# Performance work log

Hardware: AMD Instinct MI355X
Metric: run time of the kernel (lower is better)

## Reference

```python
import jax, jax.numpy as jnp
import numpy as np

DIM = 128
HEADS = 4
GN_GROUPS = 4
EPS = 1e-5


def setup_inputs() -> dict:
    key = jax.random.key(0)
    ks = jax.random.split(key, 6)
    B, C, H, W = 4, DIM, 64, 64
    x = jax.random.normal(ks[0], (B, C, H, W), dtype=jnp.float32)
    # 1x1 convs are channel matmuls: store as [out_ch, in_ch]
    w_qkv = jax.random.normal(ks[1], (3 * C, C), dtype=jnp.float32) * (C ** -0.5)
    w_out = jax.random.normal(ks[2], (C, C), dtype=jnp.float32) * (C ** -0.5)
    b_out = jax.random.normal(ks[3], (C,), dtype=jnp.float32) * 0.01
    gn_gamma = jnp.ones((C,), dtype=jnp.float32)
    gn_beta = jnp.zeros((C,), dtype=jnp.float32)
    return {"x": x, "w_qkv": w_qkv, "w_out": w_out, "b_out": b_out,
            "gn_gamma": gn_gamma, "gn_beta": gn_beta}


def _attention_block(x, w_qkv, w_out, b_out, gn_gamma, gn_beta):
    b, c, h, w = x.shape
    d = c // HEADS
    scale = d ** -0.5
    # 1x1 conv == per-pixel matmul over channels
    qkv = jnp.einsum('bchw,oc->bohw', x, w_qkv)  # [b, 3c, h, w]
    q, k, v = jnp.split(qkv, 3, axis=1)
    # 'b (h d) x y -> b h (x y) d'
    def to_heads(t):
        return t.reshape(b, HEADS, d, h * w).transpose(0, 1, 3, 2)  # [b, H, N, d]
    q, k, v = to_heads(q), to_heads(k), to_heads(v)
    dots = jnp.einsum('bhnd,bhmd->bhnm', q, k) * scale  # [b, H, N, N]
    attn = jax.nn.softmax(dots, axis=-1)
    out = jnp.einsum('bhnm,bhmd->bhnd', attn, v)  # [b, H, N, d]
    # 'b h (x y) d -> b (h d) x y'
    out = out.transpose(0, 1, 3, 2).reshape(b, c, h, w)
    # output 1x1 conv + bias
    out = jnp.einsum('bchw,oc->bohw', out, w_out) + b_out[None, :, None, None]
    # GroupNorm(4, c)
    g = out.reshape(b, GN_GROUPS, c // GN_GROUPS, h, w)
    mean = g.mean(axis=(2, 3, 4), keepdims=True)
    var = g.var(axis=(2, 3, 4), keepdims=True)
    g = (g - mean) * jax.lax.rsqrt(var + EPS)
    out = g.reshape(b, c, h, w) * gn_gamma[None, :, None, None] + gn_beta[None, :, None, None]
    return out + x


def reference(x, w_qkv, w_out, b_out, gn_gamma, gn_beta):
    return _attention_block(x, w_qkv, w_out, b_out, gn_gamma, gn_beta)
```

## Files before the change

### kernel.cpp

```cpp
#include <hip/hip_runtime.h>

#define DIM   128
#define NPIX  4096
#define DHEAD 32

using u16 = unsigned short;
typedef __attribute__((ext_vector_type(8))) short   short8;
typedef __attribute__((ext_vector_type(8))) u16     ushort8;
typedef __attribute__((ext_vector_type(4))) float   floatx4;
typedef __attribute__((ext_vector_type(2))) unsigned int uint2v;

#define SCL 0.25513899f

__device__ __forceinline__ float bf2f(u16 u) {
  union { unsigned int i; float f; } v; v.i = ((unsigned int)u) << 16; return v.f;
}
__device__ __forceinline__ u16 f2bf(float f) {
  union { unsigned int i; float f; } v; v.f = f;
  unsigned int i = v.i;
  return (u16)((i + 0x7FFFu + ((i >> 16) & 1u)) >> 16);
}
__device__ __forceinline__ unsigned int pk2bf(float a, float b) {
  union { float f; unsigned int u; } ua, ub; ua.f = a; ub.f = b;
  return __builtin_amdgcn_perm(ub.u, ua.u, 0x07060302u);
}

template<bool F32> __device__ __forceinline__ float ld1(const void* p, size_t i) {
  if constexpr (F32) return ((const float*)p)[i];
  else               return bf2f(((const u16*)p)[i]);
}
template<bool F32> __device__ __forceinline__ float4 ld4(const void* p, size_t i) {
  if constexpr (F32) {
    return *(const float4*)((const float*)p + i);
  } else {
    const ushort4 u = *(const ushort4*)((const u16*)p + i);
    return make_float4(bf2f(u.x), bf2f(u.y), bf2f(u.z), bf2f(u.w));
  }
}
template<bool F32> __device__ __forceinline__ void st4(void* p, size_t i, float4 v) {
  if constexpr (F32) {
    *(float4*)((float*)p + i) = v;
  } else {
    ushort4 u; u.x = f2bf(v.x); u.y = f2bf(v.y); u.z = f2bf(v.z); u.w = f2bf(v.w);
    *(ushort4*)((u16*)p + i) = u;
  }
}

__global__ void k_detect(const u16* __restrict__ x, int* __restrict__ flag,
                         float* __restrict__ S) {
  if (threadIdx.x < 40) S[threadIdx.x] = 0.f;
  if (threadIdx.x == 0 && blockIdx.x == 0) {
    int big = 0;
    for (int i = 0; i < 128; ++i) {
      const float v = bf2f(x[i]);
      if (!(fabsf(v) < 1e4f)) big = 1;
    }
    *flag = big;
  }
}

template<bool F32>
__global__ __launch_bounds__(256) void k_qkv(const void* __restrict__ x,
                                             const void* __restrict__ wqkv,
                                             u16* __restrict__ Q,
                                             u16* __restrict__ K,
                                             u16* __restrict__ V,
                                             const int* __restrict__ flag) {
  if (*flag != (F32 ? 1 : 0)) return;
  const int b = blockIdx.z, y = blockIdx.y, pt = blockIdx.x;
  const int tl = threadIdx.x;
  __shared__ float Ws[32 * 129];
  if (y < 8) {
    const int m = y >> 2, h = y & 3;
    const int ddq = tl & 3, pw = tl >> 2;
    const int rb = m * DIM + h * 32;
    for (int i = tl; i < 32 * DIM; i += 256)
      Ws[(i >> 7) * 129 + (i & 127)] =
          ld1<F32>(wqkv, (size_t)(rb + (i >> 7)) * DIM + (i & 127));
    __syncthreads();
    const int p0 = pt * 256 + pw * 4;
    float acc[8][4];
#pragma unroll
    for (int j = 0; j < 8; ++j) { acc[j][0] = acc[j][1] = acc[j][2] = acc[j][3] = 0.f; }
    const size_t xb = (size_t)b * DIM * NPIX + p0;
    for (int c = 0; c < DIM; ++c) {
      const float4 xv = ld4<F32>(x, xb + (size_t)c * NPIX);
#pragma unroll
      for (int j = 0; j < 8; ++j) {
        const float wv = Ws[(ddq * 8 + j) * 129 + c];
        acc[j][0] += wv * xv.x; acc[j][1] += wv * xv.y;
        acc[j][2] += wv * xv.z; acc[j][3] += wv * xv.w;
      }
    }
    u16* dst = (m == 0) ? Q : K;
    const float scl = (m == 0) ? 1.f : SCL;
    const int bh = b * 4 + h;
#pragma unroll
    for (int t = 0; t < 4; ++t) {
      ushort8 w8;
#pragma unroll
      for (int j = 0; j < 8; ++j) w8[j] = f2bf(acc[j][t] * scl);
      *(ushort8*)(dst + ((size_t)bh * NPIX + p0 + t) * DHEAD + ddq * 8) = w8;
    }
  } else {
    const int og = (y - 8) * 4 + (pt >> 2);
    const int ptv = pt & 3;
    for (int i = tl; i < 8 * DIM; i += 256)
      Ws[(i >> 7) * 129 + (i & 127)] =
          ld1<F32>(wqkv, (size_t)(2 * DIM + og * 8 + (i >> 7)) * DIM + (i & 127));
    __syncthreads();
    const int p0 = ptv * 1024 + tl * 4;
    float acc[8][4];
#pragma unroll
    for (int j = 0; j < 8; ++j) { acc[j][0] = acc[j][1] = acc[j][2] = acc[j][3] = 0.f; }
    const size_t xb = (size_t)b * DIM * NPIX + p0;
    for (int c = 0; c < DIM; ++c) {
      const float4 xv = ld4<F32>(x, xb + (size_t)c * NPIX);
#pragma unroll
      for (int j = 0; j < 8; ++j) {
        const float wv = Ws[j * 129 + c];
        acc[j][0] += wv * xv.x; acc[j][1] += wv * xv.y;
        acc[j][2] += wv * xv.z; acc[j][3] += wv * xv.w;
      }
    }
#pragma unroll
    for (int j = 0; j < 8; ++j) {
      const int c = og * 8 + j;
      ushort4 w4;
      w4.x = f2bf(acc[j][0]); w4.y = f2bf(acc[j][1]);
      w4.z = f2bf(acc[j][2]); w4.w = f2bf(acc[j][3]);
      *(ushort4*)(V + ((size_t)b * DIM + c) * NPIX + p0) = w4;
    }
  }
}

__device__ __forceinline__ short8 xform_p(unsigned c0, unsigned c1,
                                          unsigned c2, unsigned c3) {
  uint2v sw = __builtin_amdgcn_permlane32_swap(c0, c2, false, false);
  uint2v sx = __builtin_amdgcn_permlane16_swap(sw[0], sw[1], false, false);
  uint2v sy = __builtin_amdgcn_permlane32_swap(c1, c3, false, false);
  uint2v sz = __builtin_amdgcn_permlane16_swap(sy[0], sy[1], false, false);
  union { unsigned u[4]; short8 s; } r;
  r.u[0] = sx[0]; r.u[1] = sz[0]; r.u[2] = sx[1]; r.u[3] = sz[1];
  return r.s;
}

__global__ __launch_bounds__(512) void k_attn(const u16* __restrict__ Q,
                                              const u16* __restrict__ K,
                                              const u16* __restrict__ V,
                                              u16* __restrict__ O) {
  const int id = blockIdx.y * 32 + blockIdx.x;
  const int nid = (id & 7) * 64 + (id >> 3);
  const int bh = nid >> 5, qb = nid & 31;
  const int tid = threadIdx.x;
  const int wv = tid >> 6, lane = tid & 63;
  const int quad = lane >> 4, l15 = lane & 15;
  const int b = bh >> 2, h = bh & 3;

  __shared__ __align__(16) u16 Klds[2][128 * 40];
  __shared__ __align__(16) u16 Vlds[2][32 * 136];
  __shared__ __align__(16) u16 Olds[32 * 136];

  const int qtok0 = qb * 128 + wv * 16 + l15;
  const short8 qf = *(const short8*)(Q + ((size_t)bh * NPIX + qtok0) * DHEAD + quad * 8);

  floatx4 o00 = {0.f, 0.f, 0.f, 0.f}, o01 = {0.f, 0.f, 0.f, 0.f};
  floatx4 ol  = {0.f, 0.f, 0.f, 0.f};
  const short8 onesf = {(short)0x3F80, (short)0x3F80, (short)0x3F80, (short)0x3F80,
                        (short)0x3F80, (short)0x3F80, (short)0x3F80, (short)0x3F80};

  const int st = tid & 255;
  const bool isK = tid < 256;
  const int skey = st >> 2, sqt = st & 3;
  const int sdd = st >> 3, soc = st & 7;
  const u16* Gg = isK ? (K + ((size_t)bh * NPIX + skey) * DHEAD + sqt * 8)
                      : (V + ((size_t)(b * DIM + h * DHEAD + sdd)) * NPIX + soc * 8);
  u16* Ld0 = isK ? (Klds[0] + skey * 40 + sqt * 8) : (Vlds[0] + sdd * 136 + soc * 8);
  u16* Ld1 = isK ? (Klds[1] + skey * 40 + sqt * 8) : (Vlds[1] + sdd * 136 + soc * 8);
  const size_t gstep = isK ? (size_t)(128 * DHEAD) : (size_t)128;
  const size_t goff2 = isK ? (size_t)(64 * DHEAD)  : (size_t)64;
  const int    loff2 = isK ? (64 * 40) : 64;

  *(ushort8*)Ld0           = *(const ushort8*)Gg;
  *(ushort8*)(Ld0 + loff2) = *(const ushort8*)(Gg + goff2);

  for (int ch = 0; ch < 32; ++ch) {
    const int cur = ch & 1;
    __syncthreads();
    ushort8 pre0, pre1;
    if (ch + 1 < 32) {
      const u16* gb = Gg + (size_t)(ch + 1) * gstep;
      pre0 = *(const ushort8*)gb;
      pre1 = *(const ushort8*)(gb + goff2);
    }
#pragma unroll
    for (int kc = 0; kc < 4; ++kc) {
      unsigned ca[4];
#pragma unroll
      for (int s = 0; s < 2; ++s) {
        const int sub = kc * 2 + s;
        const short8 af = *(const short8*)(Klds[cur] + (sub * 16 + l15) * 40 + quad * 8);
        const floatx4 s0 = __builtin_amdgcn_mfma_f32_16x16x32_bf16(
            af, qf, (floatx4){0.f, 0.f, 0.f, 0.f}, 0, 0, 0);
        const float a0 = __builtin_amdgcn_exp2f(s0[0]);
        const float a1 = __builtin_amdgcn_exp2f(s0[1]);
        const float a2 = __builtin_amdgcn_exp2f(s0[2]);
        const float a3 = __builtin_amdgcn_exp2f(s0[3]);
        ca[s * 2 + 0] = pk2bf(a0, a1); ca[s * 2 + 1] = pk2bf(a2, a3);
      }
      const short8 pa = xform_p(ca[0], ca[1], ca[2], ca[3]);
      const short8 vb0 = *(const short8*)(Vlds[cur] + l15 * 136 + kc * 32 + quad * 8);
      const short8 vb1 = *(const short8*)(Vlds[cur] + (16 + l15) * 136 + kc * 32 + quad * 8);
      __builtin_amdgcn_s_setprio(1);
      o00 = __builtin_amdgcn_mfma_f32_16x16x32_bf16(pa, vb0, o00, 0, 0, 0);
      o01 = __builtin_amdgcn_mfma_f32_16x16x32_bf16(pa, vb1, o01, 0, 0, 0);
      ol  = __builtin_amdgcn_mfma_f32_16x16x32_bf16(pa, onesf, ol, 0, 0, 0);
      __builtin_amdgcn_s_setprio(0);
    }
    if (ch + 1 < 32) {
      u16* dst = cur ? Ld0 : Ld1;
      *(ushort8*)dst           = pre0;
      *(ushort8*)(dst + loff2) = pre1;
    }
  }
  float li[4];
#pragma unroll
  for (int r = 0; r < 4; ++r) li[r] = 1.f / ol[r];
  uint2v w00, w01;
  w00[0] = (unsigned)f2bf(o00[0] * li[0]) | ((unsigned)f2bf(o00[1] * li[1]) << 16);
  w00[1] = (unsigned)f2bf(o00[2] * li[2]) | ((unsigned)f2bf(o00[3] * li[3]) << 16);
  w01[0] = (unsigned)f2bf(o01[0] * li[0]) | ((unsigned)f2bf(o01[1] * li[1]) << 16);
  w01[1] = (unsigned)f2bf(o01[2] * li[2]) | ((unsigned)f2bf(o01[3] * li[3]) << 16);
  __syncthreads();
  *(uint2v*)(Olds + l15 * 136 + wv * 16 + quad * 4) = w00;
  *(uint2v*)(Olds + (16 + l15) * 136 + wv * 16 + quad * 4) = w01;
  __syncthreads();
  const int d = tid >> 4, oc = tid & 15;
  u16* og = O + ((size_t)(b * DIM + h * DHEAD + d)) * NPIX + qb * 128;
  *(ushort8*)(og + oc * 8) = *(const ushort8*)(Olds + d * 136 + oc * 8);
}

template<bool F32>
__global__ __launch_bounds__(256) void k_proj(const u16* __restrict__ O,
                                              const void* __restrict__ wout,
                                              const void* __restrict__ bout,
                                              float* __restrict__ Y,
                                              float* __restrict__ Sred,
                                              const int* __restrict__ flag) {
  if (*flag != (F32 ? 1 : 0)) return;
  const int b = blockIdx.z, og = blockIdx.y, pt = blockIdx.x;
  const int tl = threadIdx.x;
  __shared__ float Ws[8][DIM];
  __shared__ __align__(16) u16 Olds[2][16][520];
  for (int i = tl; i < 8 * DIM; i += 256)
    Ws[i >> 7][i & 127] = ld1<F32>(wout, (size_t)(og * 8 + (i >> 7)) * DIM + (i & 127));
  const u16* Ob = O + (size_t)b * DIM * NPIX + pt * 512;
  const int srow = tl >> 6;
  const int scol = (tl & 63) * 8;
#pragma unroll
  for (int s = 0; s < 4; ++s) {
    const int r = s * 4 + srow;
    *(ushort8*)(&Olds[0][r][scol]) = *(const ushort8*)(Ob + (size_t)r * NPIX + scol);
  }
  float acc[8][2];
#pragma unroll
  for (int j = 0; j < 8; ++j) { acc[j][0] = acc[j][1] = 0.f; }
  for (int chv = 0; chv < 8; ++chv) {
    const int cur = chv & 1;
    __syncthreads();
    ushort8 pre[4];
    if (chv + 1 < 8) {
      const u16* gb = Ob + (size_t)(chv + 1) * 16 * NPIX;
#pragma unroll
      for (int s = 0; s < 4; ++s)
        pre[s] = *(const ushort8*)(gb + (size_t)(s * 4 + srow) * NPIX + scol);
    }
#pragma unroll
    for (int cc = 0; cc < 16; ++cc) {
      const int c = chv * 16 + cc;
      const ushort2 xv2 = *(const ushort2*)(&Olds[cur][cc][tl * 2]);
      const float x0 = bf2f(xv2.x), x1 = bf2f(xv2.y);
#pragma unroll
      for (int j = 0; j < 8; ++j) {
        const float wv = Ws[j][c];
        acc[j][0] += wv * x0; acc[j][1] += wv * x1;
      }
    }
    if (chv + 1 < 8) {
      const int nxt = cur ^ 1;
#pragma unroll
      for (int s = 0; s < 4; ++s)
        *(ushort8*)(&Olds[nxt][s * 4 + srow][scol]) = pre[s];
    }
  }
  const int p0 = pt * 512 + tl * 2;
  float s1 = 0.f, s2 = 0.f;
#pragma unroll
  for (int j = 0; j < 8; ++j) {
    const int o = og * 8 + j;
    const float bo = ld1<F32>(bout, o);
    float2 y2;
    y2.x = acc[j][0] + bo; y2.y = acc[j][1] + bo;
    *(float2*)(Y + ((size_t)b * DIM + o) * NPIX + p0) = y2;
    s1 += y2.x + y2.y;
    s2 += y2.x * y2.x + y2.y * y2.y;
  }
  __shared__ float red[2][256];
  red[0][tl] = s1; red[1][tl] = s2;
  __syncthreads();
  for (int off = 128; off >= 1; off >>= 1) {
    if (tl < off) { red[0][tl] += red[0][tl + off]; red[1][tl] += red[1][tl + off]; }
    __syncthreads();
  }
  if (tl == 0) {
    const int g = og >> 2;
    atomicAdd(&Sred[(b * 4 + g) * 2 + 0], red[0][0]);
    atomicAdd(&Sred[(b * 4 + g) * 2 + 1], red[1][0]);
  }
}

template<bool F32>
__global__ __launch_bounds__(256) void k_gn(const float* __restrict__ Y,
                                            const float* __restrict__ Sred,
                                            const void* __restrict__ x,
                                            const void* __restrict__ gamma,
                                            const void* __restrict__ beta,
                                            void* __restrict__ out,
                                            const int* __restrict__ flag) {
  if (*flag != (F32 ? 1 : 0)) return;
  const int idx = (blockIdx.x * 256 + threadIdx.x) * 4;
  const int b = idx >> 19;
  const int c = (idx >> 12) & 127;
  const int g = c >> 5;
  const float inv_n = 1.f / (32.f * 4096.f);
  const float s1 = Sred[(b * 4 + g) * 2 + 0];
  const float s2 = Sred[(b * 4 + g) * 2 + 1];
  const float mean = s1 * inv_n;
  const float var = s2 * inv_n - mean * mean;
  const float rs = rsqrtf(var + 1e-5f);
  const float ga = ld1<F32>(gamma, c) * rs;
  const float be = ld1<F32>(beta, c) - mean * ga;
  const float4 y4 = *(const float4*)(Y + idx);
  const float4 xv = ld4<F32>(x, idx);
  float4 r;
  r.x = y4.x * ga + be + xv.x;
  r.y = y4.y * ga + be + xv.y;
  r.z = y4.z * ga + be + xv.z;
  r.w = y4.w * ga + be + xv.w;
  st4<F32>(out, idx, r);
}

extern "C" void kernel_launch(void* const* d_in, const int* in_sizes, int n_in,
                              void* d_out, int out_size, void* d_ws, size_t ws_size,
                              hipStream_t stream) {
  const void* x     = d_in[0];
  const void* wqkv  = d_in[1];
  const void* wout  = d_in[2];
  const void* bout  = d_in[3];
  const void* gamma = d_in[4];
  const void* beta  = d_in[5];
  char* ws = (char*)d_ws;
  u16*   Q = (u16*)(ws + ((size_t)0  << 20));
  u16*   K = (u16*)(ws + ((size_t)8  << 20));
  u16*   V = (u16*)(ws + ((size_t)16 << 20));
  u16*   O = (u16*)(ws + ((size_t)24 << 20));
  float* Y = (float*)(ws + ((size_t)32 << 20));
  float* S = (float*)(ws + ((size_t)40 << 20));
  int*   F = (int*)(ws + ((size_t)40 << 20) + 128);

  k_detect<<<1, 64, 0, stream>>>((const u16*)x, F, S);

  k_qkv<false><<<dim3(16, 12, 4), 256, 0, stream>>>(x, wqkv, Q, K, V, F);
  k_qkv<true> <<<dim3(16, 12, 4), 256, 0, stream>>>(x, wqkv, Q, K, V, F);
  k_attn<<<dim3(32, 16), 512, 0, stream>>>(Q, K, V, O);
  k_proj<false><<<dim3(8, 16, 4), 256, 0, stream>>>(O, wout, bout, Y, S, F);
  k_proj<true> <<<dim3(8, 16, 4), 256, 0, stream>>>(O, wout, bout, Y, S, F);
  k_gn<false><<<2048, 256, 0, stream>>>(Y, S, x, gamma, beta, d_out, F);
  k_gn<true> <<<2048, 256, 0, stream>>>(Y, S, x, gamma, beta, d_out, F);
}
```

Baseline: 178.5 us.

## Use MFMA bf16 tiles with double-buffered LDS staging for QKV projection

For the bf16 input path, the QKV 1x1-conv kernel now computes each 32-output by 256-pixel tile with 16x16x32 bf16 MFMA instructions instead of scalar FMAs. Weights and x are staged in padded LDS, and the next channel chunk is prefetched into registers while the current one is consumed, in a two-buffer scheme. The f32 path keeps the old scalar code. This targets the ALU cost of the projection, but the epilogue uses narrower scattered stores for V, and the grid mapping (blockIdx.y as output tile) must match the host launch, which is not shown.

Result: no change. 179.5 us (+0.5%).

```diff
diff --git a/kernel.cpp b/kernel.cpp
--- a/kernel.cpp
+++ b/kernel.cpp
@@ -67,69 +67,160 @@
                                              u16* __restrict__ V,
                                              const int* __restrict__ flag) {
   if (*flag != (F32 ? 1 : 0)) return;
-  const int b = blockIdx.z, y = blockIdx.y, pt = blockIdx.x;
+  __shared__ __align__(16) char smem[41728];
   const int tl = threadIdx.x;
-  __shared__ float Ws[32 * 129];
-  if (y < 8) {
-    const int m = y >> 2, h = y & 3;
-    const int ddq = tl & 3, pw = tl >> 2;
-    const int rb = m * DIM + h * 32;
-    for (int i = tl; i < 32 * DIM; i += 256)
-      Ws[(i >> 7) * 129 + (i & 127)] =
-          ld1<F32>(wqkv, (size_t)(rb + (i >> 7)) * DIM + (i & 127));
+  if constexpr (F32) {
+    float* Ws = (float*)smem;
+    const int b = blockIdx.z, y = blockIdx.y, pt = blockIdx.x;
+    if (y < 8) {
+      const int m = y >> 2, h = y & 3;
+      const int ddq = tl & 3, pw = tl >> 2;
+      const int rb = m * DIM + h * 32;
+      for (int i = tl; i < 32 * DIM; i += 256)
+        Ws[(i >> 7) * 129 + (i & 127)] =
+            ld1<F32>(wqkv, (size_t)(rb + (i >> 7)) * DIM + (i & 127));
+      __syncthreads();
+      const int p0 = pt * 256 + pw * 4;
+      float acc[8][4];
+#pragma unroll
+      for (int j = 0; j < 8; ++j) { acc[j][0] = acc[j][1] = acc[j][2] = acc[j][3] = 0.f; }
+      const size_t xb = (size_t)b * DIM * NPIX + p0;
+      for (int c = 0; c < DIM; ++c) {
+        const float4 xv = ld4<F32>(x, xb + (size_t)c * NPIX);
+#pragma unroll
+        for (int j = 0; j < 8; ++j) {
+          const float wv = Ws[(ddq * 8 + j) * 129 + c];
+          acc[j][0] += wv * xv.x; acc[j][1] += wv * xv.y;
+          acc[j][2] += wv * xv.z; acc[j][3] += wv * xv.w;
+        }
+      }
+      u16* dst = (m == 0) ? Q : K;
+      const float scl = (m == 0) ? 1.f : SCL;
+      const int bh = b * 4 + h;
+#pragma unroll
+      for (int t = 0; t < 4; ++t) {
+        ushort8 w8;
+#pragma unroll
+        for (int j = 0; j < 8; ++j) w8[j] = f2bf(acc[j][t] * scl);
+        *(ushort8*)(dst + ((size_t)bh * NPIX + p0 + t) * DHEAD + ddq * 8) = w8;
+      }
+    } else {
+      const int og = (y - 8) * 4 + (pt >> 2);
+      const int ptv = pt & 3;
+      for (int i = tl; i < 8 * DIM; i += 256)
+        Ws[(i >> 7) * 129 + (i & 127)] =
+            ld1<F32>(wqkv, (size_t)(2 * DIM + og * 8 + (i >> 7)) * DIM + (i & 127));
+      __syncthreads();
+      const int p0 = ptv * 1024 + tl * 4;
+      float acc[8][4];
+#pragma unroll
+      for (int j = 0; j < 8; ++j) { acc[j][0] = acc[j][1] = acc[j][2] = acc[j][3] = 0.f; }
+      const size_t xb = (size_t)b * DIM * NPIX + p0;
+      for (int c = 0; c < DIM; ++c) {
+        const float4 xv = ld4<F32>(x, xb + (size_t)c * NPIX);
+#pragma unroll
+        for (int j = 0; j < 8; ++j) {
+          const float wv = Ws[j * 129 + c];
+          acc[j][0] += wv * xv.x; acc[j][1] += wv * xv.y;
+          acc[j][2] += wv * xv.z; acc[j][3] += wv * xv.w;
+        }
+      }
+#pragma unroll
+      for (int j = 0; j < 8; ++j) {
+        const int c = og * 8 + j;
+        ushort4 w4;
+        w4.x = f2bf(acc[j][0]); w4.y = f2bf(acc[j][1]);
+        w4.z = f2bf(acc[j][2]); w4.w = f2bf(acc[j][3]);
+        *(ushort4*)(V + ((size_t)b * DIM + c) * NPIX + p0) = w4;
+      }
+    }
+  } else {
+    u16* Wl = (u16*)smem;
+    u16* Xl = (u16*)(smem + 8704);
+    const int b = blockIdx.z, ot = blockIdx.y, pt = blockIdx.x;
+    const int lane = tl & 63, wv = tl >> 6;
+    const int quad = lane >> 4, l15 = lane & 15;
+    const u16* xg = (const u16*)x;
+    const u16* wg = (const u16*)wqkv;
+    for (int i = tl; i < 32 * 16; i += 256) {
+      const int row = i >> 4, c8 = (i & 15) * 8;
+      *(ushort8*)(Wl + row * 136 + c8) =
+          *(const ushort8*)(wg + (size_t)(ot * 32 + row) * DIM + c8);
+    }
+    const int sc = tl >> 5;
+    const int sp = (tl & 31) * 8;
+    const size_t xbase = (size_t)b * DIM * NPIX + (size_t)pt * 256;
+#pragma unroll
+    for (int rr = 0; rr < 4; ++rr) {
+      const int c = rr * 8 + sc;
+      *(ushort8*)(Xl + c * 258 + sp) =
+          *(const ushort8*)(xg + xbase + (size_t)c * NPIX + sp);
+    }
     __syncthreads();
-    const int p0 = pt * 256 + pw * 4;
-    float acc[8][4];
-#pragma unroll
-    for (int j = 0; j < 8; ++j) { acc[j][0] = acc[j][1] = acc[j][2] = acc[j][3] = 0.f; }
-    const size_t xb = (size_t)b * DIM * NPIX + p0;
-    for (int c = 0; c < DIM; ++c) {
-      const float4 xv = ld4<F32>(x, xb + (size_t)c * NPIX);
-#pragma unroll
-      for (int j = 0; j < 8; ++j) {
-        const float wv = Ws[(ddq * 8 + j) * 129 + c];
-        acc[j][0] += wv * xv.x; acc[j][1] += wv * xv.y;
-        acc[j][2] += wv * xv.z; acc[j][3] += wv * xv.w;
-      }
-    }
-    u16* dst = (m == 0) ? Q : K;
-    const float scl = (m == 0) ? 1.f : SCL;
-    const int bh = b * 4 + h;
-#pragma unroll
-    for (int t = 0; t < 4; ++t) {
-      ushort8 w8;
-#pragma unroll
-      for (int j = 0; j < 8; ++j) w8[j] = f2bf(acc[j][t] * scl);
-      *(ushort8*)(dst + ((size_t)bh * NPIX + p0 + t) * DHEAD + ddq * 8) = w8;
-    }
-  } else {
-    const int og = (y - 8) * 4 + (pt >> 2);
-    const int ptv = pt & 3;
-    for (int i = tl; i < 8 * DIM; i += 256)
-      Ws[(i >> 7) * 129 + (i & 127)] =
-          ld1<F32>(wqkv, (size_t)(2 * DIM + og * 8 + (i >> 7)) * DIM + (i & 127));
-    __syncthreads();
-    const int p0 = ptv * 1024 + tl * 4;
-    float acc[8][4];
-#pragma unroll
-    for (int j = 0; j < 8; ++j) { acc[j][0] = acc[j][1] = acc[j][2] = acc[j][3] = 0.f; }
-    const size_t xb = (size_t)b * DIM * NPIX + p0;
-    for (int c = 0; c < DIM; ++c) {
-      const float4 xv = ld4<F32>(x, xb + (size_t)c * NPIX);
-#pragma unroll
-      for (int j = 0; j < 8; ++j) {
-        const float wv = Ws[j * 129 + c];
-        acc[j][0] += wv * xv.x; acc[j][1] += wv * xv.y;
-        acc[j][2] += wv * xv.z; acc[j][3] += wv * xv.w;
-      }
-    }
-#pragma unroll
-    for (int j = 0; j < 8; ++j) {
-      const int c = og * 8 + j;
-      ushort4 w4;
-      w4.x = f2bf(acc[j][0]); w4.y = f2bf(acc[j][1]);
-      w4.z = f2bf(acc[j][2]); w4.w = f2bf(acc[j][3]);
-      *(ushort4*)(V + ((size_t)b * DIM + c) * NPIX + p0) = w4;
+    short8 wf[2][4];
+#pragma unroll
+    for (int m = 0; m < 2; ++m)
+#pragma unroll
+      for (int kk = 0; kk < 4; ++kk)
+        wf[m][kk] = *(const short8*)(Wl + (m * 16 + l15) * 136 + kk * 32 + quad * 8);
+    floatx4 acc[2][4];
+#pragma unroll
+    for (int m = 0; m < 2; ++m)
+#pragma unroll
+      for (int n = 0; n < 4; ++n) acc[m][n] = (floatx4){0.f, 0.f, 0.f, 0.f};
+#pragma unroll
+    for (int kk = 0; kk < 4; ++kk) {
+      const int cur = kk & 1;
+      if (kk) __syncthreads();
+      ushort8 pre[4];
+      if (kk + 1 < 4) {
+#pragma unroll
+        for (int rr = 0; rr < 4; ++rr)
+          pre[rr] = *(const ushort8*)(
+              xg + xbase + (size_t)((kk + 1) * 32 + rr * 8 + sc) * NPIX + sp);
+      }
+#pragma unroll
+      for (int n = 0; n < 4; ++n) {
+        const int px = wv * 64 + n * 16 + l15;
+        short8 xf;
+#pragma unroll
+        for (int j = 0; j < 8; ++j)
+          xf[j] = (short)Xl[cur * (32 * 258) + (quad * 8 + j) * 258 + px];
+        acc[0][n] = __builtin_amdgcn_mfma_f32_16x16x32_bf16(wf[0][kk], xf, acc[0][n], 0, 0, 0);
+        acc[1][n] = __builtin_amdgcn_mfma_f32_16x16x32_bf16(wf[1][kk], xf, acc[1][n], 0, 0, 0);
+      }
+      if (kk + 1 < 4) {
+        u16* dst = Xl + (cur ^ 1) * (32 * 258);
+#pragma unroll
+        for (int rr = 0; rr < 4; ++rr)
+          *(ushort8*)(dst + (rr * 8 + sc) * 258 + sp) = pre[rr];
+      }
+    }
+#pragma unroll
+    for (int m = 0; m < 2; ++m) {
+      const int ob = ot * 32 + m * 16;
+      const int seg = ob >> 7;
+#pragma unroll
+      for (int n = 0; n < 4; ++n) {
+        const int px = pt * 256 + wv * 64 + n * 16 + l15;
+        if (seg < 2) {
+          const int h = (ob & 127) >> 5;
+          const int dd = (ob & 31) + quad * 4;
+          u16* dst = (seg == 0) ? Q : K;
+          const float scl = (seg == 0) ? 1.f : SCL;
+          ushort4 w4;
+          w4.x = f2bf(acc[m][n][0] * scl);
+          w4.y = f2bf(acc[m][n][1] * scl);
+          w4.z = f2bf(acc[m][n][2] * scl);
+          w4.w = f2bf(acc[m][n][3] * scl);
+          *(ushort4*)(dst + ((size_t)(b * 4 + h) * NPIX + px) * DHEAD + dd) = w4;
+        } else {
+          const int c0 = ob - 256 + quad * 4;
+#pragma unroll
+          for (int r = 0; r < 4; ++r)
+            V[((size_t)(b * DIM + c0 + r)) * NPIX + px] = f2bf(acc[m][n][r]);
+        }
+      }
     }
   }
 }
```

## Load K fragments directly from global into registers, stage only V in LDS

Applied to the files above, without the earlier changes.

The K tile is no longer staged through shared memory. Each wave now loads its K MFMA fragments directly from global memory into registers at the start of every chunk, and only V is double-buffered in LDS, with all 512 threads loading it. This removes the K LDS writes and reads and shrinks LDS use, which may raise occupancy. In exchange, every wave reads the same K data redundantly from global/L2, and the K loads are issued right before use with no prefetch, so latency may be exposed.

New measurement: 192.6 us. +7.9%, slower.

```diff
diff --git a/kernel.cpp b/kernel.cpp
--- a/kernel.cpp
+++ b/kernel.cpp
@@ -157,7 +157,6 @@
   const int quad = lane >> 4, l15 = lane & 15;
   const int b = bh >> 2, h = bh & 3;
 
-  __shared__ __align__(16) u16 Klds[2][128 * 40];
   __shared__ __align__(16) u16 Vlds[2][32 * 136];
   __shared__ __align__(16) u16 Olds[32 * 136];
 
@@ -169,39 +168,33 @@
   const short8 onesf = {(short)0x3F80, (short)0x3F80, (short)0x3F80, (short)0x3F80,
                         (short)0x3F80, (short)0x3F80, (short)0x3F80, (short)0x3F80};
 
-  const int st = tid & 255;
-  const bool isK = tid < 256;
-  const int skey = st >> 2, sqt = st & 3;
-  const int sdd = st >> 3, soc = st & 7;
-  const u16* Gg = isK ? (K + ((size_t)bh * NPIX + skey) * DHEAD + sqt * 8)
-                      : (V + ((size_t)(b * DIM + h * DHEAD + sdd)) * NPIX + soc * 8);
-  u16* Ld0 = isK ? (Klds[0] + skey * 40 + sqt * 8) : (Vlds[0] + sdd * 136 + soc * 8);
-  u16* Ld1 = isK ? (Klds[1] + skey * 40 + sqt * 8) : (Vlds[1] + sdd * 136 + soc * 8);
-  const size_t gstep = isK ? (size_t)(128 * DHEAD) : (size_t)128;
-  const size_t goff2 = isK ? (size_t)(64 * DHEAD)  : (size_t)64;
-  const int    loff2 = isK ? (64 * 40) : 64;
-
-  *(ushort8*)Ld0           = *(const ushort8*)Gg;
-  *(ushort8*)(Ld0 + loff2) = *(const ushort8*)(Gg + goff2);
+  const u16* Ka = K + ((size_t)bh * NPIX + l15) * DHEAD + quad * 8;
+
+  const int sdd = tid >> 4, soc = tid & 15;
+  const u16* Vg = V + ((size_t)(b * DIM + h * DHEAD + sdd)) * NPIX + soc * 8;
+  u16* Vd0 = Vlds[0] + sdd * 136 + soc * 8;
+  u16* Vd1 = Vlds[1] + sdd * 136 + soc * 8;
+
+  *(ushort8*)Vd0 = *(const ushort8*)Vg;
 
   for (int ch = 0; ch < 32; ++ch) {
     const int cur = ch & 1;
-    __syncthreads();
-    ushort8 pre0, pre1;
-    if (ch + 1 < 32) {
-      const u16* gb = Gg + (size_t)(ch + 1) * gstep;
-      pre0 = *(const ushort8*)gb;
-      pre1 = *(const ushort8*)(gb + goff2);
-    }
+    ushort8 kf[8];
+#pragma unroll
+    for (int sub = 0; sub < 8; ++sub)
+      kf[sub] = *(const ushort8*)(Ka + (size_t)(ch * 128 + sub * 16) * DHEAD);
+    __syncthreads();
+    ushort8 vpre;
+    if (ch + 1 < 32) vpre = *(const ushort8*)(Vg + (ch + 1) * 128);
 #pragma unroll
     for (int kc = 0; kc < 4; ++kc) {
       unsigned ca[4];
 #pragma unroll
       for (int s = 0; s < 2; ++s) {
         const int sub = kc * 2 + s;
-        const short8 af = *(const short8*)(Klds[cur] + (sub * 16 + l15) * 40 + quad * 8);
+        union { ushort8 u; short8 s8; } afc; afc.u = kf[sub];
         const floatx4 s0 = __builtin_amdgcn_mfma_f32_16x16x32_bf16(
-            af, qf, (floatx4){0.f, 0.f, 0.f, 0.f}, 0, 0, 0);
+            afc.s8, qf, (floatx4){0.f, 0.f, 0.f, 0.f}, 0, 0, 0);
         const float a0 = __builtin_amdgcn_exp2f(s0[0]);
         const float a1 = __builtin_amdgcn_exp2f(s0[1]);
         const float a2 = __builtin_amdgcn_exp2f(s0[2]);
@@ -218,9 +211,7 @@
       __builtin_amdgcn_s_setprio(0);
     }
     if (ch + 1 < 32) {
-      u16* dst = cur ? Ld0 : Ld1;
-      *(ushort8*)dst           = pre0;
-      *(ushort8*)(dst + loff2) = pre1;
+      *(ushort8*)(cur ? Vd0 : Vd1) = vpre;
     }
   }
   float li[4];
```
